# Kernel tuning notes

Hardware: AMD Instinct MI355X
Metric: run time of the kernel (lower is better)

Reference implementation:

```python
import jax, jax.numpy as jnp
import numpy as np

EPS = 1e-15
FEAT = 128
HALF = FEAT // 2
N_RBF = 20
CUTOFF = 5.0
NUM_CONV = 3
N_ATOMS = 10000
N_EDGES = 160000
N_Z = 100


def setup_inputs() -> dict:
    key = jax.random.key(0)
    ks = iter(jax.random.split(key, 40))

    def W(shape):
        fan_in = shape[-2] if len(shape) > 1 else 1
        return (jax.random.normal(next(ks), shape, jnp.float32) / np.sqrt(fan_in)).astype(jnp.float32)

    # graph
    xyz = jax.random.normal(next(ks), (N_ATOMS, 3), jnp.float32)
    z = jax.random.randint(next(ks), (N_ATOMS,), 0, N_Z)
    src = jax.random.randint(next(ks), (N_EDGES,), 0, N_ATOMS)
    off = jax.random.randint(next(ks), (N_EDGES,), 1, N_ATOMS)
    nbr_list = jnp.stack([src, (src + off) % N_ATOMS], axis=1)  # directed, no self-loops

    L = NUM_CONV
    inp = dict(
        xyz=xyz, z=z, nbr_list=nbr_list,
        embed=W((N_Z, FEAT)),
        msg_w1=W((L, FEAT, FEAT)), msg_b1=jnp.zeros((L, FEAT), jnp.float32),
        msg_w2=W((L, FEAT, 3 * FEAT)), msg_b2=jnp.zeros((L, 3 * FEAT), jnp.float32),
        dist_w=W((L, N_RBF, 3 * FEAT)), dist_b=jnp.zeros((L, 3 * FEAT), jnp.float32),
        upd_u=W((L, FEAT, FEAT)), upd_v=W((L, FEAT, FEAT)),
        upd_w1=W((L, 2 * FEAT, FEAT)), upd_b1=jnp.zeros((L, FEAT), jnp.float32),
        upd_w2=W((L, FEAT, 3 * FEAT)), upd_b2=jnp.zeros((L, 3 * FEAT), jnp.float32),
        ero_w1=W((FEAT, HALF)), ero_b1=jnp.zeros((HALF,), jnp.float32),
        ero_w2=W((HALF, 1)), ero_b2=jnp.zeros((1,), jnp.float32),
    )
    return inp


def _painn_forces(xyz, z, nbr_list, embed,
                  msg_w1, msg_b1, msg_w2, msg_b2, dist_w, dist_b,
                  upd_u, upd_v, upd_w1, upd_b1, upd_w2, upd_b2,
                  ero_w1, ero_b1, ero_w2, ero_b2):
    N = z.shape[0]
    i, j = nbr_list[:, 0], nbr_list[:, 1]
    r_ij = xyz[j] - xyz[i]                               # [E,3]
    dist = jnp.sqrt(jnp.sum(r_ij * r_ij + EPS, axis=-1))  # [E]
    unit = r_ij / dist[:, None]
    # radial basis: sin(n*pi*d/cutoff)/d, cosine cutoff envelope
    k_n = jnp.arange(1, N_RBF + 1, dtype=jnp.float32) * (np.pi / CUTOFF)
    rbf = jnp.sin(k_n * dist[:, None]) / dist[:, None]   # [E,n_rbf]
    env = jnp.where(dist < CUTOFF,
                    0.5 * (jnp.cos(np.pi * dist / CUTOFF) + 1.0), 0.0)  # [E]

    s = embed[z]                                         # [N,F]
    v = jnp.zeros((N, FEAT, 3), s.dtype)                 # [N,F,3]

    for l in range(NUM_CONV):
        # --- message block ---
        w_s = (rbf @ dist_w[l] + dist_b[l]) * env[:, None]                 # [E,3F]
        phi = jax.nn.silu(s @ msg_w1[l] + msg_b1[l]) @ msg_w2[l] + msg_b2[l]  # [N,3F]
        inv = (phi[j] * w_s).reshape(-1, 3, FEAT)                           # [E,3,F]
        dv_ij = inv[:, 0, :][..., None] * v[j] + inv[:, 2, :][..., None] * unit[:, None, :]
        ds_ij = inv[:, 1, :]
        s = s + jax.ops.segment_sum(ds_ij, i, num_segments=N)
        v = v + jax.ops.segment_sum(dv_ij, i, num_segments=N)
        # --- update block ---
        u_v = jnp.einsum('nfc,fg->ngc', v, upd_u[l])                        # [N,F,3]
        v_v = jnp.einsum('nfc,fg->ngc', v, upd_v[l])
        v_v_norm = jnp.sqrt(jnp.sum(v_v * v_v, axis=-1) + EPS)              # [N,F]
        s_stack = jnp.concatenate([s, v_v_norm], axis=-1)                   # [N,2F]
        sp = (jax.nn.silu(s_stack @ upd_w1[l] + upd_b1[l]) @ upd_w2[l] + upd_b2[l]).reshape(-1, 3, FEAT)
        v = v + u_v * sp[:, 0, :][..., None]
        s = s + jnp.sum(u_v * v_v, axis=-1) * sp[:, 1, :] + sp[:, 2, :]

    # --- edge readout -> per-atom forces ---
    e = s[i] + s[j]                                                         # [E,F]
    f_scalar = jax.nn.silu(e @ ero_w1 + ero_b1) @ ero_w2 + ero_b2           # [E,1]
    dis_vec = xyz[i] - xyz[j]
    dis = jnp.sqrt(jnp.sum(dis_vec * dis_vec, axis=1))[:, None]
    f_edge = f_scalar * (dis_vec / dis)                                     # [E,3]
    f_atom = (jax.ops.segment_sum(f_edge, i, num_segments=N)
              - jax.ops.segment_sum(f_edge, j, num_segments=N))             # [N,3]
    return f_atom


def reference(xyz, z, nbr_list, embed,
              msg_w1, msg_b1, msg_w2, msg_b2, dist_w, dist_b,
              upd_u, upd_v, upd_w1, upd_b1, upd_w2, upd_b2,
              ero_w1, ero_b1, ero_w2, ero_b2):
    return _painn_forces(xyz, z, nbr_list, embed,
                         msg_w1, msg_b1, msg_w2, msg_b2, dist_w, dist_b,
                         upd_u, upd_v, upd_w1, upd_b1, upd_w2, upd_b2,
                         ero_w1, ero_b1, ero_w2, ero_b2)
```

## Files before the change

### kernel.cpp

```cpp
#include <hip/hip_runtime.h>
#include <math.h>

#define EPS_F 1e-15f
#define NRBF 20
#define CUTOFF_F 5.0f
#define PI_F 3.14159265358979323846f

typedef unsigned short u16;
typedef _Float16 f16;
typedef f16 f16x8 __attribute__((ext_vector_type(8)));
typedef f16 f16x4 __attribute__((ext_vector_type(4)));
typedef float floatx4 __attribute__((ext_vector_type(4)));

__device__ __forceinline__ float silu_f(float x) { return x / (1.0f + expf(-x)); }

__global__ __launch_bounds__(256) void hist_kernel(
    const int* __restrict__ nbr, int* __restrict__ hist, int E)
{
  int e = blockIdx.x * 256 + threadIdx.x;
  if (e >= E) return;
  atomicAdd(hist + nbr[2 * e], 1);
}

__global__ __launch_bounds__(1024) void scan_kernel(
    const int* __restrict__ hist, int* __restrict__ start,
    int* __restrict__ cursor, int N)
{
  __shared__ int wsum[16];
  __shared__ int carry_s;
  int tid = threadIdx.x;
  int lane = tid & 63, wid = tid >> 6;
  if (tid == 0) carry_s = 0;
  __syncthreads();
  for (int base = 0; base < N; base += 1024) {
    int x = (base + tid < N) ? hist[base + tid] : 0;
    int v = x;
#pragma unroll
    for (int o = 1; o < 64; o <<= 1) {
      int t2 = __shfl_up(v, o, 64);
      if (lane >= o) v += t2;
    }
    if (lane == 63) wsum[wid] = v;
    __syncthreads();
    if (tid < 16) {
      int w = wsum[tid];
#pragma unroll
      for (int o = 1; o < 16; o <<= 1) {
        int t2 = __shfl_up(w, o, 64);
        if (tid >= o) w += t2;
      }
      wsum[tid] = w;
    }
    __syncthreads();
    int wbase = (wid == 0) ? 0 : wsum[wid - 1];
    int incl = v + wbase;
    int carry = carry_s;
    if (base + tid < N) {
      int ex = carry + incl - x;
      start[base + tid] = ex;
      cursor[base + tid] = ex;
    }
    __syncthreads();
    if (tid == 1023) carry_s = carry + incl;
    __syncthreads();
  }
  if (tid == 0) start[N] = carry_s;
}

__global__ __launch_bounds__(256) void scatter_id_kernel(
    const int* __restrict__ nbr, int* __restrict__ cursor,
    int* __restrict__ order, int E)
{
  int e = blockIdx.x * 256 + threadIdx.x;
  if (e >= E) return;
  int pos = atomicAdd(cursor + nbr[2 * e], 1);
  order[pos] = e;
}

__global__ __launch_bounds__(256) void segsort_kernel(
    int* __restrict__ order, const int* __restrict__ start, int N)
{
  int wi = blockIdx.x * 4 + (threadIdx.x >> 6);
  int lane = threadIdx.x & 63;
  if (wi >= N) return;
  int s0 = start[wi], s1 = start[wi + 1];
  int len = s1 - s0;
  if (len <= 1) return;
  if (len <= 64) {
    int id = (lane < len) ? order[s0 + lane] : 0x7FFFFFFF;
    int rank = 0;
#pragma unroll
    for (int k = 0; k < 64; ++k) {
      int other = __shfl(id, k, 64);
      rank += (other < id) ? 1 : 0;
    }
    if (lane < len) order[s0 + rank] = id;
  } else if (lane == 0) {
    for (int a = s0 + 1; a < s1; ++a) {
      int key = order[a];
      int b = a - 1;
      while (b >= s0 && order[b] > key) { order[b + 1] = order[b]; --b; }
      order[b + 1] = key;
    }
  }
}

__global__ __launch_bounds__(256) void geom_fill_kernel(
    const int* __restrict__ order, const int* __restrict__ nbr,
    const float* __restrict__ xyz, int* __restrict__ nbrj_s,
    float* __restrict__ unit_s, float* __restrict__ env_s,
    f16* __restrict__ rbf_h, int E)
{
  int p = blockIdx.x * 256 + threadIdx.x;
  if (p >= E) return;
  int e = order[p];
  int i = nbr[2 * e], j = nbr[2 * e + 1];
  float dx = xyz[3 * j + 0] - xyz[3 * i + 0];
  float dy = xyz[3 * j + 1] - xyz[3 * i + 1];
  float dz = xyz[3 * j + 2] - xyz[3 * i + 2];
  float d2 = dx * dx + dy * dy + dz * dz + 3.0f * EPS_F;
  float d = sqrtf(d2);
  float inv_d = 1.0f / d;
  nbrj_s[p] = j;
  unit_s[3 * p + 0] = dx * inv_d;
  unit_s[3 * p + 1] = dy * inv_d;
  unit_s[3 * p + 2] = dz * inv_d;
  float x = d * (PI_F / CUTOFF_F);
  float s1, c1;
  __sincosf(x, &s1, &c1);
  env_s[p] = (d < CUTOFF_F) ? 0.5f * (c1 + 1.0f) : 0.0f;
  f16 tmp[32];
  float two_c = 2.0f * c1;
  float sp = 0.0f, sn = s1;
  tmp[0] = (f16)(sn * inv_d);
#pragma unroll
  for (int n = 1; n < NRBF; ++n) {
    float nx = two_c * sn - sp;
    sp = sn; sn = nx;
    tmp[n] = (f16)(sn * inv_d);
  }
#pragma unroll
  for (int n = NRBF; n < 32; ++n) tmp[n] = (f16)0.0f;
#pragma unroll
  for (int g = 0; g < 4; ++g)
    *(f16x8*)(rbf_h + (size_t)p * 32 + g * 8) = *(f16x8*)&tmp[g * 8];
}

__global__ __launch_bounds__(256) void embed_kernel(
    const int* __restrict__ z, const float* __restrict__ embed,
    float* __restrict__ s, f16* __restrict__ s_h, int N)
{
  int idx = blockIdx.x * 256 + threadIdx.x;
  if (idx >= N * 128) return;
  int n = idx >> 7, f = idx & 127;
  float x = embed[z[n] * 128 + f];
  s[idx] = x;
  s_h[idx] = (f16)x;
}

__global__ __launch_bounds__(256) void w1t_kernel(
    const float* __restrict__ w1, f16* __restrict__ w1t)
{
  int idx = blockIdx.x * 256 + threadIdx.x;
  if (idx >= 64 * 128) return;
  int n = idx >> 7, k = idx & 127;
  w1t[idx] = (f16)w1[(size_t)k * 64 + n];
}

#define WS_EPB 32
__global__ __launch_bounds__(256) void ws_kernel(
    const f16* __restrict__ rbf_h, const float* __restrict__ env_s,
    const float* __restrict__ dw, const float* __restrict__ db,
    f16* __restrict__ ws_out, int Mc)
{
  __shared__ float dwL[NRBF][384];
  __shared__ float dbL[384];
  int t = threadIdx.x;
  for (int idx = t; idx < NRBF * 384 / 4; idx += 256)
    ((float4*)&dwL[0][0])[idx] = ((const float4*)dw)[idx];
  for (int idx = t; idx < 384; idx += 256) dbL[idx] = db[idx];
  __syncthreads();
  int w = t >> 6, lane = t & 63;
  int e_loc = lane >> 3, cg_loc = lane & 7;
  int e = blockIdx.x * WS_EPB + w * 8 + e_loc;
  bool ok = e < Mc;
  float rb[NRBF];
  float env = 0.f;
  if (ok) {
    const f16* rp = rbf_h + (size_t)e * 32;
#pragma unroll
    for (int k = 0; k < NRBF; ++k) rb[k] = (float)rp[k];
    env = env_s[e];
  }
#pragma unroll
  for (int itc = 0; itc < 6; ++itc) {
    int col = (itc * 8 + cg_loc) * 8;
    float acc[8];
    *(float4*)&acc[0] = *(const float4*)&dbL[col];
    *(float4*)&acc[4] = *(const float4*)&dbL[col + 4];
#pragma unroll
    for (int k = 0; k < NRBF; ++k) {
      float4 d0 = *(const float4*)&dwL[k][col];
      float4 d1 = *(const float4*)&dwL[k][col + 4];
      float r = rb[k];
      acc[0] = fmaf(r, d0.x, acc[0]); acc[1] = fmaf(r, d0.y, acc[1]);
      acc[2] = fmaf(r, d0.z, acc[2]); acc[3] = fmaf(r, d0.w, acc[3]);
      acc[4] = fmaf(r, d1.x, acc[4]); acc[5] = fmaf(r, d1.y, acc[5]);
      acc[6] = fmaf(r, d1.z, acc[6]); acc[7] = fmaf(r, d1.w, acc[7]);
    }
    if (ok) {
      f16x8 o;
#pragma unroll
      for (int q = 0; q < 8; ++q) o[q] = (f16)(acc[q] * env);
      *(f16x8*)(ws_out + (size_t)e * 384 + col) = o;
    }
  }
}

template <bool SILU, int OUT, bool AH>
__global__ __launch_bounds__(256) void gemm_kernel(
    const void* __restrict__ Ap, const float* __restrict__ W,
    const float* __restrict__ bias, const float* __restrict__ rowscale,
    void* __restrict__ Cout, int M, int N, int K)
{
  __shared__ f16 As[64][40];
  __shared__ f16 Bs[64][40];
  int t = threadIdx.x;
  int wave = t >> 6, lane = t & 63;
  int rw = wave & 1, cw = wave >> 1;
  int lr = lane & 15, quad = lane >> 4;
  int row0 = blockIdx.x * 64, col0 = blockIdx.y * 64;
  floatx4 acc[2][2] = {};
  for (int k0 = 0; k0 < K; k0 += 32) {
    if (AH) {
      const f16* A = (const f16*)Ap;
      int sm = t >> 2, sk = (t & 3) * 8;
      f16x8 av;
      if (row0 + sm < M) av = *(const f16x8*)(A + (size_t)(row0 + sm) * K + k0 + sk);
      else { for (int q = 0; q < 8; ++q) av[q] = (f16)0.0f; }
      *(f16x8*)&As[sm][sk] = av;
    } else {
      const float* A = (const float*)Ap;
#pragma unroll
      for (int u0 = 0; u0 < 2; ++u0) {
        int u = t + u0 * 256;
        int m = u >> 3, c4 = (u & 7) * 4;
        float4 av = make_float4(0.f, 0.f, 0.f, 0.f);
        if (row0 + m < M) av = *(const float4*)(A + (size_t)(row0 + m) * K + k0 + c4);
        f16x4 hv;
        hv[0] = (f16)av.x; hv[1] = (f16)av.y; hv[2] = (f16)av.z; hv[3] = (f16)av.w;
        *(f16x4*)&As[m][c4] = hv;
      }
    }
#pragma unroll
    for (int u0 = 0; u0 < 2; ++u0) {
      int u = t + u0 * 256;
      int k = u >> 4, n4 = (u & 15) * 4;
      float4 wv = *(const float4*)(W + (size_t)(k0 + k) * N + col0 + n4);
      Bs[n4 + 0][k] = (f16)wv.x;
      Bs[n4 + 1][k] = (f16)wv.y;
      Bs[n4 + 2][k] = (f16)wv.z;
      Bs[n4 + 3][k] = (f16)wv.w;
    }
    __syncthreads();
    f16x8 af[2], bfr[2];
#pragma unroll
    for (int tr = 0; tr < 2; ++tr)
      af[tr] = *(const f16x8*)&As[rw * 32 + tr * 16 + lr][quad * 8];
#pragma unroll
    for (int tc = 0; tc < 2; ++tc)
      bfr[tc] = *(const f16x8*)&Bs[cw * 32 + tc * 16 + lr][quad * 8];
#pragma unroll
    for (int tr = 0; tr < 2; ++tr)
#pragma unroll
      for (int tc = 0; tc < 2; ++tc)
        acc[tr][tc] = __builtin_amdgcn_mfma_f32_16x16x32_f16(af[tr], bfr[tc], acc[tr][tc], 0, 0, 0);
    __syncthreads();
  }
#pragma unroll
  for (int tc = 0; tc < 2; ++tc) {
    int col = col0 + cw * 32 + tc * 16 + lr;
    float bb = bias ? bias[col] : 0.0f;
#pragma unroll
    for (int tr = 0; tr < 2; ++tr) {
#pragma unroll
      for (int r = 0; r < 4; ++r) {
        int row = row0 + rw * 32 + tr * 16 + quad * 4 + r;
        if (row < M) {
          float x = acc[tr][tc][r] + bb;
          if (rowscale) x *= rowscale[row];
          if (SILU) x = silu_f(x);
          size_t o = (size_t)row * N + col;
          if (OUT == 0) ((float*)Cout)[o] = x;
          else          ((f16*)Cout)[o] = (f16)x;
        }
      }
    }
  }
}

__global__ __launch_bounds__(256) void gemm_dual_kernel(
    const float* __restrict__ A, const float* __restrict__ W1,
    const float* __restrict__ W2, float* __restrict__ C1, float* __restrict__ C2,
    int M, int N, int K)
{
  __shared__ f16 As[64][40];
  __shared__ f16 Bs1[64][40];
  __shared__ f16 Bs2[64][40];
  int t = threadIdx.x;
  int wave = t >> 6, lane = t & 63;
  int rw = wave & 1, cw = wave >> 1;
  int lr = lane & 15, quad = lane >> 4;
  int row0 = blockIdx.x * 64, col0 = blockIdx.y * 64;
  floatx4 acc1[2][2] = {};
  floatx4 acc2[2][2] = {};
  for (int k0 = 0; k0 < K; k0 += 32) {
#pragma unroll
    for (int u0 = 0; u0 < 2; ++u0) {
      int u = t + u0 * 256;
      int m = u >> 3, c4 = (u & 7) * 4;
      float4 av = make_float4(0.f, 0.f, 0.f, 0.f);
      if (row0 + m < M) av = *(const float4*)(A + (size_t)(row0 + m) * K + k0 + c4);
      f16x4 hv;
      hv[0] = (f16)av.x; hv[1] = (f16)av.y; hv[2] = (f16)av.z; hv[3] = (f16)av.w;
      *(f16x4*)&As[m][c4] = hv;
    }
#pragma unroll
    for (int u0 = 0; u0 < 2; ++u0) {
      int u = t + u0 * 256;
      int k = u >> 4, n4 = (u & 15) * 4;
      float4 wv = *(const float4*)(W1 + (size_t)(k0 + k) * N + col0 + n4);
      Bs1[n4 + 0][k] = (f16)wv.x;
      Bs1[n4 + 1][k] = (f16)wv.y;
      Bs1[n4 + 2][k] = (f16)wv.z;
      Bs1[n4 + 3][k] = (f16)wv.w;
      float4 xv = *(const float4*)(W2 + (size_t)(k0 + k) * N + col0 + n4);
      Bs2[n4 + 0][k] = (f16)xv.x;
      Bs2[n4 + 1][k] = (f16)xv.y;
      Bs2[n4 + 2][k] = (f16)xv.z;
      Bs2[n4 + 3][k] = (f16)xv.w;
    }
    __syncthreads();
    f16x8 af[2], b1[2], b2[2];
#pragma unroll
    for (int tr = 0; tr < 2; ++tr)
      af[tr] = *(const f16x8*)&As[rw * 32 + tr * 16 + lr][quad * 8];
#pragma unroll
    for (int tc = 0; tc < 2; ++tc) {
      b1[tc] = *(const f16x8*)&Bs1[cw * 32 + tc * 16 + lr][quad * 8];
      b2[tc] = *(const f16x8*)&Bs2[cw * 32 + tc * 16 + lr][quad * 8];
    }
#pragma unroll
    for (int tr = 0; tr < 2; ++tr)
#pragma unroll
      for (int tc = 0; tc < 2; ++tc) {
        acc1[tr][tc] = __builtin_amdgcn_mfma_f32_16x16x32_f16(af[tr], b1[tc], acc1[tr][tc], 0, 0, 0);
        acc2[tr][tc] = __builtin_amdgcn_mfma_f32_16x16x32_f16(af[tr], b2[tc], acc2[tr][tc], 0, 0, 0);
      }
    __syncthreads();
  }
#pragma unroll
  for (int tc = 0; tc < 2; ++tc) {
    int col = col0 + cw * 32 + tc * 16 + lr;
#pragma unroll
    for (int tr = 0; tr < 2; ++tr) {
#pragma unroll
      for (int r = 0; r < 4; ++r) {
        int row = row0 + rw * 32 + tr * 16 + quad * 4 + r;
        if (row < M) {
          C1[(size_t)row * N + col] = acc1[tr][tc][r];
          C2[(size_t)row * N + col] = acc2[tr][tc][r];
        }
      }
    }
  }
}

__global__ __launch_bounds__(512) void message_kernel(
    const int* __restrict__ nbrj_s, const float* __restrict__ unit_s,
    const f16* __restrict__ wsb, const f16* __restrict__ phi_h,
    const f16* __restrict__ vh_in, const float* __restrict__ v_in,
    float* __restrict__ s, float* __restrict__ v_out,
    const int* __restrict__ start, int N, int e_lo, int e_hi, int first)
{
  __shared__ float part[3][4][128];
  int i = blockIdx.x;
  int t = threadIdx.x;
  int f = t & 127, h = t >> 7;
  int e0 = start[i], e1 = start[i + 1];
  if (e0 < e_lo) e0 = e_lo;
  if (e1 > e_hi) e1 = e_hi;
  bool active = e1 > e0;
  if (!first && !active) return;
  int len = active ? (e1 - e0) : 0;
  int me0 = e0 + (len * h) / 4;
  int me1 = e0 + (len * (h + 1)) / 4;
  float acc_s = 0.f, av0 = 0.f, av1 = 0.f, av2 = 0.f;
#pragma unroll 2
  for (int e = me0; e < me1; ++e) {
    int j = nbrj_s[e];
    const f16* wsr = wsb + (size_t)(e - e_lo) * 384;
    float ws0 = (float)wsr[f];
    float ws1 = (float)wsr[128 + f];
    float ws2 = (float)wsr[256 + f];
    const f16* ph = phi_h + (size_t)j * 384;
    float inv0 = (float)ph[f] * ws0;
    float inv1 = (float)ph[128 + f] * ws1;
    float inv2 = (float)ph[256 + f] * ws2;
    float ux = unit_s[3 * e + 0], uy = unit_s[3 * e + 1], uz = unit_s[3 * e + 2];
    const f16* vj = vh_in + (size_t)j * 384;
    acc_s += inv1;
    av0 = fmaf(inv0, (float)vj[f],       fmaf(inv2, ux, av0));
    av1 = fmaf(inv0, (float)vj[128 + f], fmaf(inv2, uy, av1));
    av2 = fmaf(inv0, (float)vj[256 + f], fmaf(inv2, uz, av2));
  }
  if (h >= 1) {
    part[h - 1][0][f] = acc_s;
    part[h - 1][1][f] = av0;
    part[h - 1][2][f] = av1;
    part[h - 1][3][f] = av2;
  }
  __syncthreads();
  if (h == 0) {
#pragma unroll
    for (int q = 0; q < 3; ++q) {
      acc_s += part[q][0][f];
      av0   += part[q][1][f];
      av1   += part[q][2][f];
      av2   += part[q][3][f];
    }
    if (active) s[(size_t)i * 128 + f] += acc_s;
    size_t o = (size_t)i * 384 + f;
    if (first) {
      v_out[o]       = v_in[o]       + av0;
      v_out[o + 128] = v_in[o + 128] + av1;
      v_out[o + 256] = v_in[o + 256] + av2;
    } else {
      v_out[o]       += av0;
      v_out[o + 128] += av1;
      v_out[o + 256] += av2;
    }
  }
}

__global__ __launch_bounds__(256) void stack_kernel(
    const float* __restrict__ s, const float* __restrict__ v_v,
    f16* __restrict__ s_stack, int N)
{
  int idx = blockIdx.x * 256 + threadIdx.x;
  if (idx >= N * 128) return;
  int n = idx >> 7, g = idx & 127;
  float a = v_v[(size_t)n * 384 + g];
  float b = v_v[(size_t)n * 384 + 128 + g];
  float c = v_v[(size_t)n * 384 + 256 + g];
  s_stack[(size_t)n * 256 + g] = (f16)s[idx];
  s_stack[(size_t)n * 256 + 128 + g] = (f16)sqrtf(a * a + b * b + c * c + EPS_F);
}

__global__ __launch_bounds__(256) void apply_kernel(
    float* __restrict__ s, f16* __restrict__ s_h,
    float* __restrict__ v, f16* __restrict__ v_h,
    const float* __restrict__ u_v, const float* __restrict__ v_v,
    const float* __restrict__ sp, int N)
{
  int idx = blockIdx.x * 256 + threadIdx.x;
  if (idx >= N * 128) return;
  int n = idx >> 7, g = idx & 127;
  float sp0 = sp[(size_t)n * 384 + g];
  float sp1 = sp[(size_t)n * 384 + 128 + g];
  float sp2 = sp[(size_t)n * 384 + 256 + g];
  float dot = 0.f;
#pragma unroll
  for (int c = 0; c < 3; ++c) {
    size_t o = (size_t)n * 384 + c * 128 + g;
    float uv = u_v[o];
    float vn = fmaf(uv, sp0, v[o]);
    v[o] = vn;
    v_h[o] = (f16)vn;
    dot = fmaf(uv, v_v[o], dot);
  }
  float sn = s[idx] + dot * sp1 + sp2;
  s[idx] = sn;
  s_h[idx] = (f16)sn;
}

__global__ __launch_bounds__(256) void readout_gemm_kernel(
    const int* __restrict__ nbr, const float* __restrict__ xyz,
    const f16* __restrict__ s_h, const f16* __restrict__ w1t,
    const float* __restrict__ b1, const float* __restrict__ w2,
    const float* __restrict__ b2, float* __restrict__ out, int E)
{
  __shared__ f16 As[64][40];
  __shared__ f16 Bs[64][40];
  __shared__ float red[2][64];
  __shared__ int ijc[64][2];
  int t = threadIdx.x;
  int wave = t >> 6, lane = t & 63;
  int rw = wave & 1, cw = wave >> 1;
  int lr = lane & 15, quad = lane >> 4;
  int e0b = blockIdx.x * 64;
  if (t < 64) {
    int e = e0b + t;
    if (e < E) { ijc[t][0] = nbr[2 * e]; ijc[t][1] = nbr[2 * e + 1]; }
    else { ijc[t][0] = 0; ijc[t][1] = 0; }
  }
  __syncthreads();
  int m = t >> 2;
  int c8 = (t & 3) * 8;
  int im = ijc[m][0], jm = ijc[m][1];
  bool okm = (e0b + m) < E;
  f16x8 xa[4], ya[4];
  if (okm) {
#pragma unroll
    for (int w = 0; w < 4; ++w) {
      xa[w] = *(const f16x8*)(s_h + (size_t)im * 128 + w * 32 + c8);
      ya[w] = *(const f16x8*)(s_h + (size_t)jm * 128 + w * 32 + c8);
    }
  } else {
#pragma unroll
    for (int w = 0; w < 4; ++w)
      for (int q = 0; q < 8; ++q) { xa[w][q] = (f16)0.0f; ya[w][q] = (f16)0.0f; }
  }
  floatx4 acc[2][2] = {};
#pragma unroll
  for (int w = 0; w < 4; ++w) {
    *(f16x8*)&As[m][c8] = xa[w] + ya[w];
    {
      int sm = t >> 2, sk = (t & 3) * 8;
      *(f16x8*)&Bs[sm][sk] = *(const f16x8*)(w1t + (size_t)sm * 128 + w * 32 + sk);
    }
    __syncthreads();
    f16x8 af[2], bfr[2];
#pragma unroll
    for (int tr = 0; tr < 2; ++tr)
      af[tr] = *(const f16x8*)&As[rw * 32 + tr * 16 + lr][quad * 8];
#pragma unroll
    for (int tc = 0; tc < 2; ++tc)
      bfr[tc] = *(const f16x8*)&Bs[cw * 32 + tc * 16 + lr][quad * 8];
#pragma unroll
    for (int tr = 0; tr < 2; ++tr)
#pragma unroll
      for (int tc = 0; tc < 2; ++tc)
        acc[tr][tc] = __builtin_amdgcn_mfma_f32_16x16x32_f16(af[tr], bfr[tc], acc[tr][tc], 0, 0, 0);
    __syncthreads();
  }
  float b1v[2], w2v[2];
#pragma unroll
  for (int tc = 0; tc < 2; ++tc) {
    int col = cw * 32 + tc * 16 + lr;
    b1v[tc] = b1[col];
    w2v[tc] = w2[col];
  }
#pragma unroll
  for (int tr = 0; tr < 2; ++tr) {
#pragma unroll
    for (int r = 0; r < 4; ++r) {
      float p = 0.f;
#pragma unroll
      for (int tc = 0; tc < 2; ++tc)
        p += silu_f(acc[tr][tc][r] + b1v[tc]) * w2v[tc];
#pragma unroll
      for (int ofs = 1; ofs < 16; ofs <<= 1) p += __shfl_xor(p, ofs, 64);
      if (lr == 0) red[cw][rw * 32 + tr * 16 + quad * 4 + r] = p;
    }
  }
  __syncthreads();
  if (t < 64) {
    int e = e0b + t;
    if (e < E) {
      float fs = red[0][t] + red[1][t] + b2[0];
      int i = ijc[t][0], j = ijc[t][1];
      float dx = xyz[3 * i + 0] - xyz[3 * j + 0];
      float dy = xyz[3 * i + 1] - xyz[3 * j + 1];
      float dz = xyz[3 * i + 2] - xyz[3 * j + 2];
      float dis = sqrtf(dx * dx + dy * dy + dz * dz);
      float sc = fs / dis;
      float fx = sc * dx, fy = sc * dy, fz = sc * dz;
      atomicAdd(out + (size_t)i * 3 + 0, fx);
      atomicAdd(out + (size_t)i * 3 + 1, fy);
      atomicAdd(out + (size_t)i * 3 + 2, fz);
      atomicAdd(out + (size_t)j * 3 + 0, -fx);
      atomicAdd(out + (size_t)j * 3 + 1, -fy);
      atomicAdd(out + (size_t)j * 3 + 2, -fz);
    }
  }
}

extern "C" void kernel_launch(void* const* d_in, const int* in_sizes, int n_in,
                              void* d_out, int out_size, void* d_ws, size_t ws_size,
                              hipStream_t stream) {
  const float* xyz    = (const float*)d_in[0];
  const int*   z      = (const int*)d_in[1];
  const int*   nbr    = (const int*)d_in[2];
  const float* embed  = (const float*)d_in[3];
  const float* msg_w1 = (const float*)d_in[4];
  const float* msg_b1 = (const float*)d_in[5];
  const float* msg_w2 = (const float*)d_in[6];
  const float* msg_b2 = (const float*)d_in[7];
  const float* dist_w = (const float*)d_in[8];
  const float* dist_b = (const float*)d_in[9];
  const float* upd_u  = (const float*)d_in[10];
  const float* upd_v  = (const float*)d_in[11];
  const float* upd_w1 = (const float*)d_in[12];
  const float* upd_b1 = (const float*)d_in[13];
  const float* upd_w2 = (const float*)d_in[14];
  const float* upd_b2 = (const float*)d_in[15];
  const float* ero_w1 = (const float*)d_in[16];
  const float* ero_b1 = (const float*)d_in[17];
  const float* ero_w2 = (const float*)d_in[18];
  const float* ero_b2 = (const float*)d_in[19];

  const int N = in_sizes[1];
  const int E = in_sizes[2] / 2;
  const int L = 3;

  char* ws = (char*)d_ws;
  size_t off = 0;
  auto alloc = [&](size_t bytes) -> void* {
    void* p = ws + off;
    off += (bytes + 255) & ~(size_t)255;
    return p;
  };
  float* unit_s = (float*)alloc((size_t)E * 3 * 4);
  float* env_s  = (float*)alloc((size_t)E * 4);
  f16*   rbf_h  = (f16*)alloc((size_t)E * 32 * 2);
  int*   nbrj_s = (int*)alloc((size_t)E * 4);
  int*   order  = (int*)alloc((size_t)E * 4);
  float* s      = (float*)alloc((size_t)N * 128 * 4);
  f16*   s_h    = (f16*)alloc((size_t)N * 128 * 2);
  float* vA     = (float*)alloc((size_t)N * 384 * 4);
  float* vB     = (float*)alloc((size_t)N * 384 * 4);
  f16*   vhA    = (f16*)alloc((size_t)N * 384 * 2);
  f16*   vhB    = (f16*)alloc((size_t)N * 384 * 2);
  f16*   phi_h  = (f16*)alloc((size_t)N * 384 * 2);
  f16*   w1t    = (f16*)alloc((size_t)64 * 128 * 2);
  int*   histx  = (int*)alloc((size_t)(N + 1) * 4);
  int*   startp = (int*)alloc((size_t)(N + 1) * 4);
  int*   cursor = (int*)alloc((size_t)N * 4);
  size_t ovl_base = off;
  float* u_v    = (float*)alloc((size_t)N * 384 * 4);
  float* v_v    = (float*)alloc((size_t)N * 384 * 4);
  float* sp     = (float*)alloc((size_t)N * 384 * 4);
  f16*   sstk_h = (f16*)alloc((size_t)N * 256 * 2);
  f16*   h_h    = (f16*)alloc((size_t)N * 128 * 2);
  f16*   ws_buf = (f16*)((char*)d_ws + ovl_base);

  auto cdiv = [](int a, int b) { return (a + b - 1) / b; };
  int C = 1;
  {
    size_t cap = (ws_size > ovl_base) ? ws_size - ovl_base : 0;
    while (C < 32) {
      size_t need = (size_t)cdiv(E, C) * 384 * 2 + 512;
      if (need <= cap) break;
      C <<= 1;
    }
  }
  int ecl = cdiv(E, C);

  hipMemsetAsync(vA, 0, (size_t)N * 384 * 4, stream);
  hipMemsetAsync(vhA, 0, (size_t)N * 384 * 2, stream);
  hipMemsetAsync(histx, 0, (size_t)(N + 1) * 4, stream);
  hist_kernel<<<cdiv(E, 256), 256, 0, stream>>>(nbr, histx, E);
  scan_kernel<<<1, 1024, 0, stream>>>(histx, startp, cursor, N);
  scatter_id_kernel<<<cdiv(E, 256), 256, 0, stream>>>(nbr, cursor, order, E);
  segsort_kernel<<<cdiv(N, 4), 256, 0, stream>>>(order, startp, N);
  geom_fill_kernel<<<cdiv(E, 256), 256, 0, stream>>>(
      order, nbr, xyz, nbrj_s, unit_s, env_s, rbf_h, E);
  embed_kernel<<<cdiv(N * 128, 256), 256, 0, stream>>>(z, embed, s, s_h, N);
  w1t_kernel<<<cdiv(64 * 128, 256), 256, 0, stream>>>(ero_w1, w1t);

  float* v_cur = vA;  float* v_nxt = vB;
  f16*   vh_cur = vhA; f16*  vh_nxt = vhB;
  for (int l = 0; l < L; ++l) {
    gemm_kernel<true, 1, true><<<dim3(cdiv(N, 64), 2), 256, 0, stream>>>(
        s_h, msg_w1 + (size_t)l * 128 * 128, msg_b1 + (size_t)l * 128, nullptr, h_h, N, 128, 128);
    gemm_kernel<false, 1, true><<<dim3(cdiv(N, 64), 6), 256, 0, stream>>>(
        h_h, msg_w2 + (size_t)l * 128 * 384, msg_b2 + (size_t)l * 384, nullptr, phi_h, N, 384, 128);
    for (int c = 0; c < C; ++c) {
      int elo = c * ecl, ehi = (elo + ecl < E) ? elo + ecl : E;
      int Mc = ehi - elo;
      if (Mc <= 0) continue;
      ws_kernel<<<cdiv(Mc, WS_EPB), 256, 0, stream>>>(
          rbf_h + (size_t)elo * 32, env_s + elo,
          dist_w + (size_t)l * NRBF * 384, dist_b + (size_t)l * 384, ws_buf, Mc);
      message_kernel<<<N, 512, 0, stream>>>(
          nbrj_s, unit_s, ws_buf, phi_h, vh_cur, v_cur, s, v_nxt, startp,
          N, elo, ehi, c == 0);
    }
    float* v = v_nxt;
    gemm_dual_kernel<<<dim3(cdiv(N * 3, 64), 2), 256, 0, stream>>>(
        v, upd_u + (size_t)l * 128 * 128, upd_v + (size_t)l * 128 * 128,
        u_v, v_v, N * 3, 128, 128);
    stack_kernel<<<cdiv(N * 128, 256), 256, 0, stream>>>(s, v_v, sstk_h, N);
    gemm_kernel<true, 1, true><<<dim3(cdiv(N, 64), 2), 256, 0, stream>>>(
        sstk_h, upd_w1 + (size_t)l * 256 * 128, upd_b1 + (size_t)l * 128, nullptr, h_h, N, 128, 256);
    gemm_kernel<false, 0, true><<<dim3(cdiv(N, 64), 6), 256, 0, stream>>>(
        h_h, upd_w2 + (size_t)l * 128 * 384, upd_b2 + (size_t)l * 384, nullptr, sp, N, 384, 128);
    apply_kernel<<<cdiv(N * 128, 256), 256, 0, stream>>>(
        s, s_h, v, vh_nxt, u_v, v_v, sp, N);
    v_cur = v_nxt;   v_nxt = (v_cur == vA) ? vB : vA;
    f16* th = vh_cur; vh_cur = vh_nxt; vh_nxt = th;
  }

  hipMemsetAsync(d_out, 0, (size_t)out_size * 4, stream);
  readout_gemm_kernel<<<cdiv(E, 64), 256, 0, stream>>>(
      nbr, xyz, s_h, w1t, ero_b1, ero_w2, ero_b2, (float*)d_out, E);
}
```

Before: 772.9 us.

## Fuse RBF distance filter projection into message kernel, drop ws buffer

Folds the cosine envelope into the stored RBF values and adds the envelope as a 21st basis entry so the bias gets scaled correctly. The message kernel now keeps the per-feature distance weights in registers and computes the three filter values per edge on the fly. This removes the separate ws_kernel, its E×384 fp16 intermediate buffer and the edge chunking loop. In exchange each message thread does about 63 extra FMAs per edge and holds many more registers, and launch bounds now request 4 blocks per CU.

```diff
diff --git a/kernel.cpp b/kernel.cpp
--- a/kernel.cpp
+++ b/kernel.cpp
@@ -108,8 +108,7 @@
 __global__ __launch_bounds__(256) void geom_fill_kernel(
     const int* __restrict__ order, const int* __restrict__ nbr,
     const float* __restrict__ xyz, int* __restrict__ nbrj_s,
-    float* __restrict__ unit_s, float* __restrict__ env_s,
-    f16* __restrict__ rbf_h, int E)
+    float* __restrict__ unit_s, f16* __restrict__ rbf_h, int E)
 {
   int p = blockIdx.x * 256 + threadIdx.x;
   if (p >= E) return;
@@ -128,19 +127,21 @@
   float x = d * (PI_F / CUTOFF_F);
   float s1, c1;
   __sincosf(x, &s1, &c1);
-  env_s[p] = (d < CUTOFF_F) ? 0.5f * (c1 + 1.0f) : 0.0f;
+  float envv = (d < CUTOFF_F) ? 0.5f * (c1 + 1.0f) : 0.0f;
   f16 tmp[32];
   float two_c = 2.0f * c1;
+  float env_inv_d = envv * inv_d;
   float sp = 0.0f, sn = s1;
-  tmp[0] = (f16)(sn * inv_d);
+  tmp[0] = (f16)(sn * env_inv_d);
 #pragma unroll
   for (int n = 1; n < NRBF; ++n) {
     float nx = two_c * sn - sp;
     sp = sn; sn = nx;
-    tmp[n] = (f16)(sn * inv_d);
-  }
-#pragma unroll
-  for (int n = NRBF; n < 32; ++n) tmp[n] = (f16)0.0f;
+    tmp[n] = (f16)(sn * env_inv_d);
+  }
+  tmp[NRBF] = (f16)envv;
+#pragma unroll
+  for (int n = NRBF + 1; n < 32; ++n) tmp[n] = (f16)0.0f;
 #pragma unroll
   for (int g = 0; g < 4; ++g)
     *(f16x8*)(rbf_h + (size_t)p * 32 + g * 8) = *(f16x8*)&tmp[g * 8];
@@ -165,56 +166,6 @@
   if (idx >= 64 * 128) return;
   int n = idx >> 7, k = idx & 127;
   w1t[idx] = (f16)w1[(size_t)k * 64 + n];
-}
-
-#define WS_EPB 32
-__global__ __launch_bounds__(256) void ws_kernel(
-    const f16* __restrict__ rbf_h, const float* __restrict__ env_s,
-    const float* __restrict__ dw, const float* __restrict__ db,
-    f16* __restrict__ ws_out, int Mc)
-{
-  __shared__ float dwL[NRBF][384];
-  __shared__ float dbL[384];
-  int t = threadIdx.x;
-  for (int idx = t; idx < NRBF * 384 / 4; idx += 256)
-    ((float4*)&dwL[0][0])[idx] = ((const float4*)dw)[idx];
-  for (int idx = t; idx < 384; idx += 256) dbL[idx] = db[idx];
-  __syncthreads();
-  int w = t >> 6, lane = t & 63;
-  int e_loc = lane >> 3, cg_loc = lane & 7;
-  int e = blockIdx.x * WS_EPB + w * 8 + e_loc;
-  bool ok = e < Mc;
-  float rb[NRBF];
-  float env = 0.f;
-  if (ok) {
-    const f16* rp = rbf_h + (size_t)e * 32;
-#pragma unroll
-    for (int k = 0; k < NRBF; ++k) rb[k] = (float)rp[k];
-    env = env_s[e];
-  }
-#pragma unroll
-  for (int itc = 0; itc < 6; ++itc) {
-    int col = (itc * 8 + cg_loc) * 8;
-    float acc[8];
-    *(float4*)&acc[0] = *(const float4*)&dbL[col];
-    *(float4*)&acc[4] = *(const float4*)&dbL[col + 4];
-#pragma unroll
-    for (int k = 0; k < NRBF; ++k) {
-      float4 d0 = *(const float4*)&dwL[k][col];
-      float4 d1 = *(const float4*)&dwL[k][col + 4];
-      float r = rb[k];
-      acc[0] = fmaf(r, d0.x, acc[0]); acc[1] = fmaf(r, d0.y, acc[1]);
-      acc[2] = fmaf(r, d0.z, acc[2]); acc[3] = fmaf(r, d0.w, acc[3]);
-      acc[4] = fmaf(r, d1.x, acc[4]); acc[5] = fmaf(r, d1.y, acc[5]);
-      acc[6] = fmaf(r, d1.z, acc[6]); acc[7] = fmaf(r, d1.w, acc[7]);
-    }
-    if (ok) {
-      f16x8 o;
-#pragma unroll
-      for (int q = 0; q < 8; ++q) o[q] = (f16)(acc[q] * env);
-      *(f16x8*)(ws_out + (size_t)e * 384 + col) = o;
-    }
-  }
 }
 
 template <bool SILU, int OUT, bool AH>
@@ -376,33 +327,53 @@
   }
 }
 
-__global__ __launch_bounds__(512) void message_kernel(
+__global__ __launch_bounds__(512, 4) void message_kernel(
     const int* __restrict__ nbrj_s, const float* __restrict__ unit_s,
-    const f16* __restrict__ wsb, const f16* __restrict__ phi_h,
+    const f16* __restrict__ rbf_h, const float* __restrict__ dw,
+    const float* __restrict__ db, const f16* __restrict__ phi_h,
     const f16* __restrict__ vh_in, const float* __restrict__ v_in,
     float* __restrict__ s, float* __restrict__ v_out,
-    const int* __restrict__ start, int N, int e_lo, int e_hi, int first)
+    const int* __restrict__ start, int N)
 {
   __shared__ float part[3][4][128];
   int i = blockIdx.x;
   int t = threadIdx.x;
   int f = t & 127, h = t >> 7;
+  float dwc[NRBF + 1][3];
+#pragma unroll
+  for (int k = 0; k < NRBF; ++k) {
+    dwc[k][0] = dw[k * 384 + f];
+    dwc[k][1] = dw[k * 384 + 128 + f];
+    dwc[k][2] = dw[k * 384 + 256 + f];
+  }
+  dwc[NRBF][0] = db[f];
+  dwc[NRBF][1] = db[128 + f];
+  dwc[NRBF][2] = db[256 + f];
   int e0 = start[i], e1 = start[i + 1];
-  if (e0 < e_lo) e0 = e_lo;
-  if (e1 > e_hi) e1 = e_hi;
-  bool active = e1 > e0;
-  if (!first && !active) return;
-  int len = active ? (e1 - e0) : 0;
+  int len = e1 - e0;
   int me0 = e0 + (len * h) / 4;
   int me1 = e0 + (len * (h + 1)) / 4;
   float acc_s = 0.f, av0 = 0.f, av1 = 0.f, av2 = 0.f;
-#pragma unroll 2
   for (int e = me0; e < me1; ++e) {
     int j = nbrj_s[e];
-    const f16* wsr = wsb + (size_t)(e - e_lo) * 384;
-    float ws0 = (float)wsr[f];
-    float ws1 = (float)wsr[128 + f];
-    float ws2 = (float)wsr[256 + f];
+    const f16* rp = rbf_h + (size_t)e * 32;
+    f16x8 r0 = *(const f16x8*)rp;
+    f16x8 r1 = *(const f16x8*)(rp + 8);
+    f16x8 r2 = *(const f16x8*)(rp + 16);
+    float rb[NRBF + 1];
+#pragma unroll
+    for (int q = 0; q < 8; ++q) rb[q] = (float)r0[q];
+#pragma unroll
+    for (int q = 0; q < 8; ++q) rb[8 + q] = (float)r1[q];
+#pragma unroll
+    for (int q = 0; q < 5; ++q) rb[16 + q] = (float)r2[q];
+    float ws0 = 0.f, ws1 = 0.f, ws2 = 0.f;
+#pragma unroll
+    for (int k = 0; k <= NRBF; ++k) {
+      ws0 = fmaf(rb[k], dwc[k][0], ws0);
+      ws1 = fmaf(rb[k], dwc[k][1], ws1);
+      ws2 = fmaf(rb[k], dwc[k][2], ws2);
+    }
     const f16* ph = phi_h + (size_t)j * 384;
     float inv0 = (float)ph[f] * ws0;
     float inv1 = (float)ph[128 + f] * ws1;
@@ -429,17 +400,11 @@
       av1   += part[q][2][f];
       av2   += part[q][3][f];
     }
-    if (active) s[(size_t)i * 128 + f] += acc_s;
+    s[(size_t)i * 128 + f] += acc_s;
     size_t o = (size_t)i * 384 + f;
-    if (first) {
-      v_out[o]       = v_in[o]       + av0;
-      v_out[o + 128] = v_in[o + 128] + av1;
-      v_out[o + 256] = v_in[o + 256] + av2;
-    } else {
-      v_out[o]       += av0;
-      v_out[o + 128] += av1;
-      v_out[o + 256] += av2;
-    }
+    v_out[o]       = v_in[o]       + av0;
+    v_out[o + 128] = v_in[o + 128] + av1;
+    v_out[o + 256] = v_in[o + 256] + av2;
   }
 }
 
@@ -622,7 +587,6 @@
     return p;
   };
   float* unit_s = (float*)alloc((size_t)E * 3 * 4);
-  float* env_s  = (float*)alloc((size_t)E * 4);
   f16*   rbf_h  = (f16*)alloc((size_t)E * 32 * 2);
   int*   nbrj_s = (int*)alloc((size_t)E * 4);
   int*   order  = (int*)alloc((size_t)E * 4);
@@ -637,25 +601,13 @@
   int*   histx  = (int*)alloc((size_t)(N + 1) * 4);
   int*   startp = (int*)alloc((size_t)(N + 1) * 4);
   int*   cursor = (int*)alloc((size_t)N * 4);
-  size_t ovl_base = off;
   float* u_v    = (float*)alloc((size_t)N * 384 * 4);
   float* v_v    = (float*)alloc((size_t)N * 384 * 4);
   float* sp     = (float*)alloc((size_t)N * 384 * 4);
   f16*   sstk_h = (f16*)alloc((size_t)N * 256 * 2);
   f16*   h_h    = (f16*)alloc((size_t)N * 128 * 2);
-  f16*   ws_buf = (f16*)((char*)d_ws + ovl_base);
 
   auto cdiv = [](int a, int b) { return (a + b - 1) / b; };
-  int C = 1;
-  {
-    size_t cap = (ws_size > ovl_base) ? ws_size - ovl_base : 0;
-    while (C < 32) {
-      size_t need = (size_t)cdiv(E, C) * 384 * 2 + 512;
-      if (need <= cap) break;
-      C <<= 1;
-    }
-  }
-  int ecl = cdiv(E, C);
 
   hipMemsetAsync(vA, 0, (size_t)N * 384 * 4, stream);
   hipMemsetAsync(vhA, 0, (size_t)N * 384 * 2, stream);
@@ -665,7 +617,7 @@
   scatter_id_kernel<<<cdiv(E, 256), 256, 0, stream>>>(nbr, cursor, order, E);
   segsort_kernel<<<cdiv(N, 4), 256, 0, stream>>>(order, startp, N);
   geom_fill_kernel<<<cdiv(E, 256), 256, 0, stream>>>(
-      order, nbr, xyz, nbrj_s, unit_s, env_s, rbf_h, E);
+      order, nbr, xyz, nbrj_s, unit_s, rbf_h, E);
   embed_kernel<<<cdiv(N * 128, 256), 256, 0, stream>>>(z, embed, s, s_h, N);
   w1t_kernel<<<cdiv(64 * 128, 256), 256, 0, stream>>>(ero_w1, w1t);
 
@@ -676,17 +628,10 @@
         s_h, msg_w1 + (size_t)l * 128 * 128, msg_b1 + (size_t)l * 128, nullptr, h_h, N, 128, 128);
     gemm_kernel<false, 1, true><<<dim3(cdiv(N, 64), 6), 256, 0, stream>>>(
         h_h, msg_w2 + (size_t)l * 128 * 384, msg_b2 + (size_t)l * 384, nullptr, phi_h, N, 384, 128);
-    for (int c = 0; c < C; ++c) {
-      int elo = c * ecl, ehi = (elo + ecl < E) ? elo + ecl : E;
-      int Mc = ehi - elo;
-      if (Mc <= 0) continue;
-      ws_kernel<<<cdiv(Mc, WS_EPB), 256, 0, stream>>>(
-          rbf_h + (size_t)elo * 32, env_s + elo,
-          dist_w + (size_t)l * NRBF * 384, dist_b + (size_t)l * 384, ws_buf, Mc);
-      message_kernel<<<N, 512, 0, stream>>>(
-          nbrj_s, unit_s, ws_buf, phi_h, vh_cur, v_cur, s, v_nxt, startp,
-          N, elo, ehi, c == 0);
-    }
+    message_kernel<<<N, 512, 0, stream>>>(
+        nbrj_s, unit_s, rbf_h,
+        dist_w + (size_t)l * NRBF * 384, dist_b + (size_t)l * 384,
+        phi_h, vh_cur, v_cur, s, v_nxt, startp, N);
     float* v = v_nxt;
     gemm_dual_kernel<<<dim3(cdiv(N * 3, 64), 2), 256, 0, stream>>>(
         v, upd_u + (size_t)l * 128 * 128, upd_v + (size_t)l * 128 * 128,
```

Result: slower. 1.021 ms (+32.2%).
